# Optimization experiments

Hardware: AMD Instinct MI355X
Metric: run time of the kernel (lower is better)

The kernel has to match this reference:

```python
import jax, jax.numpy as jnp
import numpy as np

N = 50000
E = 800000


def gcn_conv(h_in, W, b, src, dst, n_nodes):
    # h_in: [N, Fin] -> linear transform first (PyG GCNConv default)
    h = h_in @ W  # [N, Fout]
    # add self loops
    loop = jnp.arange(n_nodes, dtype=src.dtype)
    s = jnp.concatenate([src, loop])
    d = jnp.concatenate([dst, loop])
    # symmetric normalization: deg computed on destination with unit edge weights
    deg = jax.ops.segment_sum(jnp.ones_like(s, dtype=h.dtype), d, num_segments=n_nodes)
    dinv = jnp.where(deg > 0, jax.lax.rsqrt(deg), 0.0)
    norm = dinv[s] * dinv[d]  # [E+N]
    # gather source features, scale, scatter-add to destinations
    msg = h[s] * norm[:, None]  # [E+N, Fout]
    out = jax.ops.segment_sum(msg, d, num_segments=n_nodes)
    return out + b


def setup_inputs() -> dict:
    key = jax.random.key(0)
    ks = jax.random.split(key, 6)
    x = jax.random.normal(ks[0], (N, 256), dtype=jnp.float32)
    edge_index = jax.random.randint(ks[1], (2, E), 0, N, dtype=jnp.int64)
    # Glorot-style scaling for weights
    W1 = jax.random.normal(ks[2], (256, 128), dtype=jnp.float32) * (1.0 / np.sqrt(256))
    b1 = jnp.zeros((128,), dtype=jnp.float32)
    W2 = jax.random.normal(ks[3], (128, 64), dtype=jnp.float32) * (1.0 / np.sqrt(128))
    b2 = jnp.zeros((64,), dtype=jnp.float32)
    return {"x": x, "edge_index": edge_index, "W1": W1, "b1": b1, "W2": W2, "b2": b2}


def reference(x, edge_index, W1, b1, W2, b2):
    src, dst = edge_index[0], edge_index[1]
    h = gcn_conv(x, W1, b1, src, dst, N)
    h = jax.nn.relu(h)
    out = gcn_conv(h, W2, b2, src, dst, N)
    return out
```

## Files before the change

kernel.cpp:

```cpp
#include <hip/hip_runtime.h>

#define FIN   256
#define F1    128
#define F2    64

typedef _Float16 f16x8 __attribute__((ext_vector_type(8)));
typedef _Float16 f16x4 __attribute__((ext_vector_type(4)));
typedef float    f32x4 __attribute__((ext_vector_type(4)));

#define BUCKET_SHIFT 7
#define BUCKET_W     128
#define MAXBUCK      512
#define CAP          2560
#define CHUNK        2048

__global__ __launch_bounds__(256) void prep(const float* __restrict__ W1,
                                            const float* __restrict__ W2,
                                            _Float16* __restrict__ WT1,
                                            _Float16* __restrict__ WT2,
                                            int* __restrict__ bcur_pad) {
    int b = blockIdx.x;
    if (b == 0) {
        for (int i = threadIdx.x; i < MAXBUCK; i += 256) bcur_pad[i * 16] = i * CAP;
        return;
    }
    int idx = (b - 1) * 256 + threadIdx.x;
    if (idx < FIN * F1) {
        int k = idx / F1, n = idx % F1;
        WT1[(size_t)n * FIN + k] = (_Float16)W1[idx];
    } else {
        int j = idx - FIN * F1;
        if (j < F1 * F2) {
            int k = j / F2, n = j % F2;
            WT2[(size_t)n * F1 + k] = (_Float16)W2[j];
        }
    }
}

__global__ __launch_bounds__(512) void bucket_fill(const int* __restrict__ src,
                                                   const int* __restrict__ dst,
                                                   int* __restrict__ bcur_pad,
                                                   unsigned* __restrict__ ebuf, int E) {
    __shared__ int h[MAXBUCK];
    __shared__ int base[MAXBUCK];
    for (int i = threadIdx.x; i < MAXBUCK; i += 512) h[i] = 0;
    __syncthreads();
    int cbase = blockIdx.x * CHUNK;
    int lim   = min(cbase + CHUNK, E);
    for (int e = cbase + threadIdx.x; e < lim; e += 512)
        atomicAdd(&h[dst[e] >> BUCKET_SHIFT], 1);
    __syncthreads();
    for (int i = threadIdx.x; i < MAXBUCK; i += 512) {
        int c = h[i];
        base[i] = c ? atomicAdd(&bcur_pad[i * 16], c) : 0;
        h[i] = 0;
    }
    __syncthreads();
    for (int e = cbase + threadIdx.x; e < lim; e += 512) {
        int d = dst[e], b = d >> BUCKET_SHIFT;
        int r = atomicAdd(&h[b], 1);
        int pos = base[b] + r;
        if (pos < (b + 1) * CAP)
            ebuf[pos] = ((unsigned)src[e] << BUCKET_SHIFT) | (unsigned)(d & (BUCKET_W - 1));
    }
}

__global__ __launch_bounds__(512) void csr_build(const unsigned* __restrict__ ebuf,
                                                 const int* __restrict__ bcur_pad,
                                                 unsigned* __restrict__ rowinfo,
                                                 float* __restrict__ dinv,
                                                 int* __restrict__ csr, int n) {
    __shared__ int cnt[BUCKET_W];
    __shared__ int sbuf[2][BUCKET_W];
    __shared__ int lcur[BUCKET_W];
    int k = blockIdx.x, t = threadIdx.x;
    int ebeg = k * CAP;
    int cntk = min(bcur_pad[k * 16] - ebeg, CAP);
    if (t < BUCKET_W) cnt[t] = 0;
    __syncthreads();
    for (int e = t; e < cntk; e += 512)
        atomicAdd(&cnt[ebuf[ebeg + e] & (BUCKET_W - 1)], 1);
    __syncthreads();
    int myc = (t < BUCKET_W) ? cnt[t] : 0;
    if (t < BUCKET_W) sbuf[0][t] = myc;
    __syncthreads();
    int cur = 0;
    for (int off = 1; off < BUCKET_W; off <<= 1) {
        if (t < BUCKET_W) {
            int v = sbuf[cur][t];
            if (t >= off) v += sbuf[cur][t - off];
            sbuf[cur ^ 1][t] = v;
        }
        cur ^= 1;
        __syncthreads();
    }
    if (t < BUCKET_W) {
        int excl = sbuf[cur][t] - myc;
        int beg  = ebeg + excl;
        lcur[t] = beg;
        int node = (k << BUCKET_SHIFT) + t;
        if (node < n) {
            rowinfo[node] = ((unsigned)beg << 8) | (unsigned)min(myc, 255);
            dinv[node]    = rsqrtf((float)(myc + 1));
        }
    }
    __syncthreads();
    for (int e = t; e < cntk; e += 512) {
        unsigned ed = ebuf[ebeg + e];
        int pos = atomicAdd(&lcur[ed & (BUCKET_W - 1)], 1);
        csr[pos] = (int)(ed >> BUCKET_SHIFT);
    }
}

template <int BN, int K, typename AT>
__global__ __launch_bounds__(256) void gemm_mfma(const AT* __restrict__ A,
                                                 const _Float16* __restrict__ WT,
                                                 const float* __restrict__ dinv,
                                                 _Float16* __restrict__ Ch, int M) {
    constexpr int NB = BN / 16;
    constexpr int CH = K / 32;
    constexpr int KP = K + 8;
    __shared__ _Float16 Bs[BN][KP];

    int tid  = threadIdx.x;
    int wave = tid >> 6, lane = tid & 63;
    int col  = lane & 15, kg = lane >> 4;
    int row0 = blockIdx.x * 64;
    int arow = row0 + wave * 16 + col;
    bool rowok = arow < M;

    float4 paf[sizeof(AT) == 4 ? 2 * CH : 1];
    f16x8  pah[sizeof(AT) == 2 ? CH : 1];
    const AT* Ab = A + (size_t)arow * K + kg * 8;
    if constexpr (sizeof(AT) == 4) {
#pragma unroll
        for (int c = 0; c < CH; ++c) {
            paf[2 * c]     = make_float4(0.f, 0.f, 0.f, 0.f);
            paf[2 * c + 1] = make_float4(0.f, 0.f, 0.f, 0.f);
            if (rowok) {
                paf[2 * c]     = *(const float4*)((const float*)Ab + c * 32);
                paf[2 * c + 1] = *(const float4*)((const float*)Ab + c * 32 + 4);
            }
        }
    } else {
#pragma unroll
        for (int c = 0; c < CH; ++c) {
            pah[c] = (f16x8){0, 0, 0, 0, 0, 0, 0, 0};
            if (rowok) pah[c] = *(const f16x8*)((const _Float16*)Ab + c * 32);
        }
    }

    constexpr int TOT = BN * K / 8;
#pragma unroll
    for (int l = 0; l < TOT / 256; ++l) {
        int u  = l * 256 + tid;
        int r  = u / (K / 8);
        int c8 = u % (K / 8);
        *(f16x8*)&Bs[r][c8 * 8] = *(const f16x8*)&WT[(size_t)r * K + c8 * 8];
    }
    __syncthreads();

    f32x4 acc[NB];
#pragma unroll
    for (int j = 0; j < NB; ++j) acc[j] = (f32x4){0.f, 0.f, 0.f, 0.f};

#pragma unroll
    for (int c = 0; c < CH; ++c) {
        f16x8 a;
        if constexpr (sizeof(AT) == 4) {
            float4 lo = paf[2 * c], hi = paf[2 * c + 1];
            a[0] = (_Float16)lo.x; a[1] = (_Float16)lo.y;
            a[2] = (_Float16)lo.z; a[3] = (_Float16)lo.w;
            a[4] = (_Float16)hi.x; a[5] = (_Float16)hi.y;
            a[6] = (_Float16)hi.z; a[7] = (_Float16)hi.w;
        } else {
            a = pah[c];
        }
#pragma unroll
        for (int j = 0; j < NB; ++j) {
            f16x8 b = *(const f16x8*)&Bs[j * 16 + col][c * 32 + kg * 8];
            acc[j] = __builtin_amdgcn_mfma_f32_16x16x32_f16(a, b, acc[j], 0, 0, 0);
        }
    }

    int rbase = row0 + wave * 16 + kg * 4;
#pragma unroll
    for (int r = 0; r < 4; ++r) {
        int m = rbase + r;
        if (m < M) {
            float dv = dinv[m];
#pragma unroll
            for (int j = 0; j < NB; ++j)
                Ch[(size_t)m * BN + j * 16 + col] = (_Float16)(dv * acc[j][r]);
        }
    }
}

template <int F, bool RELU, typename OutT>
__global__ __launch_bounds__(256) void aggregate(const _Float16* __restrict__ Hs,
                                                 const unsigned* __restrict__ rowinfo,
                                                 const int* __restrict__ csr,
                                                 const float* __restrict__ dinv,
                                                 const float* __restrict__ bias,
                                                 OutT* __restrict__ out, int n) {
    constexpr int LPG = F / 8;
    int gid = (blockIdx.x * blockDim.x + threadIdx.x) / LPG;
    int sub = threadIdx.x & (LPG - 1);
    if (gid >= n) return;
    const int col = sub * 8;

    float a[8];
    {
        f16x8 h = *(const f16x8*)&Hs[(size_t)gid * F + col];
#pragma unroll
        for (int i = 0; i < 8; ++i) a[i] = (float)h[i];
    }

    unsigned ri = rowinfo[gid];
    int e   = (int)(ri >> 8);
    int end = e + (int)(ri & 255u);

    for (; e + 8 <= end; e += 8) {
        int s0 = csr[e + 0], s1 = csr[e + 1], s2 = csr[e + 2], s3 = csr[e + 3];
        int s4 = csr[e + 4], s5 = csr[e + 5], s6 = csr[e + 6], s7 = csr[e + 7];
        f16x8 v0 = *(const f16x8*)&Hs[(size_t)s0 * F + col];
        f16x8 v1 = *(const f16x8*)&Hs[(size_t)s1 * F + col];
        f16x8 v2 = *(const f16x8*)&Hs[(size_t)s2 * F + col];
        f16x8 v3 = *(const f16x8*)&Hs[(size_t)s3 * F + col];
        f16x8 v4 = *(const f16x8*)&Hs[(size_t)s4 * F + col];
        f16x8 v5 = *(const f16x8*)&Hs[(size_t)s5 * F + col];
        f16x8 v6 = *(const f16x8*)&Hs[(size_t)s6 * F + col];
        f16x8 v7 = *(const f16x8*)&Hs[(size_t)s7 * F + col];
#pragma unroll
        for (int i = 0; i < 8; ++i) {
            a[i] += (((float)v0[i] + (float)v1[i]) + ((float)v2[i] + (float)v3[i]))
                  + (((float)v4[i] + (float)v5[i]) + ((float)v6[i] + (float)v7[i]));
        }
    }
    for (; e + 4 <= end; e += 4) {
        int s0 = csr[e + 0], s1 = csr[e + 1], s2 = csr[e + 2], s3 = csr[e + 3];
        f16x8 v0 = *(const f16x8*)&Hs[(size_t)s0 * F + col];
        f16x8 v1 = *(const f16x8*)&Hs[(size_t)s1 * F + col];
        f16x8 v2 = *(const f16x8*)&Hs[(size_t)s2 * F + col];
        f16x8 v3 = *(const f16x8*)&Hs[(size_t)s3 * F + col];
#pragma unroll
        for (int i = 0; i < 8; ++i)
            a[i] += ((float)v0[i] + (float)v1[i]) + ((float)v2[i] + (float)v3[i]);
    }
    for (; e < end; ++e) {
        int s = csr[e];
        f16x8 v = *(const f16x8*)&Hs[(size_t)s * F + col];
#pragma unroll
        for (int i = 0; i < 8; ++i) a[i] += (float)v[i];
    }

    float dv = dinv[gid];
    float4 bb0 = *(const float4*)&bias[col];
    float4 bb1 = *(const float4*)&bias[col + 4];
    float o[8];
    o[0] = dv * a[0] + bb0.x; o[1] = dv * a[1] + bb0.y;
    o[2] = dv * a[2] + bb0.z; o[3] = dv * a[3] + bb0.w;
    o[4] = dv * a[4] + bb1.x; o[5] = dv * a[5] + bb1.y;
    o[6] = dv * a[6] + bb1.z; o[7] = dv * a[7] + bb1.w;
    if (RELU) {
#pragma unroll
        for (int i = 0; i < 8; ++i) o[i] = fmaxf(o[i], 0.f);
    }
    if constexpr (sizeof(OutT) == 2) {
        f16x8 ov;
#pragma unroll
        for (int i = 0; i < 8; ++i) ov[i] = (_Float16)o[i];
        *(f16x8*)&out[(size_t)gid * F + col] = ov;
    } else {
        float4 ov0 = make_float4(o[0], o[1], o[2], o[3]);
        float4 ov1 = make_float4(o[4], o[5], o[6], o[7]);
        *(float4*)&out[(size_t)gid * F + col]     = ov0;
        *(float4*)&out[(size_t)gid * F + col + 4] = ov1;
    }
}

extern "C" void kernel_launch(void* const* d_in, const int* in_sizes, int n_in,
                              void* d_out, int out_size, void* d_ws, size_t ws_size,
                              hipStream_t stream) {
    const float* x  = (const float*)d_in[0];
    const int*   ei = (const int*)d_in[1];
    const float* W1 = (const float*)d_in[2];
    const float* b1 = (const float*)d_in[3];
    const float* W2 = (const float*)d_in[4];
    const float* b2 = (const float*)d_in[5];
    float* out = (float*)d_out;

    const int N = in_sizes[0] / FIN;
    const int E = in_sizes[1] / 2;
    const int* src = ei;
    const int* dst = ei + E;

    char* w = (char*)d_ws;
    auto alloc = [&](size_t bytes) {
        void* p = (void*)w;
        w += (bytes + 255) & ~(size_t)255;
        return p;
    };
    float*    dinv     = (float*)alloc((size_t)N * 4);
    unsigned* rowinfo  = (unsigned*)alloc((size_t)N * 4);
    int*      csr      = (int*)alloc((size_t)MAXBUCK * CAP * 4);
    int*      bcur_pad = (int*)alloc((size_t)MAXBUCK * 16 * 4);
    unsigned* ebuf     = (unsigned*)alloc((size_t)MAXBUCK * CAP * 4);
    _Float16* WT1      = (_Float16*)alloc((size_t)FIN * F1 * 2);
    _Float16* WT2      = (_Float16*)alloc((size_t)F1 * F2 * 2);
    _Float16* Hs1      = (_Float16*)alloc((size_t)N * F1 * 2);
    _Float16* X2h      = (_Float16*)alloc((size_t)N * F1 * 2);

    const int nbuck  = (N + BUCKET_W - 1) >> BUCKET_SHIFT;
    const int nchunk = (E + CHUNK - 1) / CHUNK;
    const int nprep  = 1 + (FIN * F1 + F1 * F2 + 255) / 256;

    prep<<<nprep, 256, 0, stream>>>(W1, W2, WT1, WT2, bcur_pad);
    bucket_fill<<<nchunk, 512, 0, stream>>>(src, dst, bcur_pad, ebuf, E);
    csr_build<<<nbuck, 512, 0, stream>>>(ebuf, bcur_pad, rowinfo, dinv, csr, N);

    gemm_mfma<F1, FIN, float><<<(N + 63) / 64, 256, 0, stream>>>(x, WT1, dinv, Hs1, N);
    {
        int blocks = (int)(((size_t)N * (F1 / 8) + 255) / 256);
        aggregate<F1, true, _Float16><<<blocks, 256, 0, stream>>>(Hs1, rowinfo, csr, dinv, b1, X2h, N);
    }

    gemm_mfma<F2, F1, _Float16><<<(N + 63) / 64, 256, 0, stream>>>(X2h, WT2, dinv, Hs1, N);
    {
        int blocks = (int)(((size_t)N * (F2 / 8) + 255) / 256);
        aggregate<F2, false, float><<<blocks, 256, 0, stream>>>(Hs1, rowinfo, csr, dinv, b2, out, N);
    }
}
```

Measured before the change: 109.8 us.

## Fuse layer-1 aggregation with layer-2 GEMM in one kernel

Replaces the separate layer-1 aggregate kernel and layer-2 MFMA GEMM with a single kernel. Each 64-node block aggregates neighbours into shared memory, applies bias and ReLU, then multiplies by W2 with MFMA and writes the dinv-scaled fp16 result. This avoids writing and re-reading the N x 128 fp16 intermediate and saves one kernel launch. In exchange, each block uses more shared memory and runs the gather and the GEMM back to back without overlap.

```diff
diff --git a/kernel.cpp b/kernel.cpp
--- a/kernel.cpp
+++ b/kernel.cpp
@@ -192,6 +192,125 @@
 #pragma unroll
             for (int j = 0; j < NB; ++j)
                 Ch[(size_t)m * BN + j * 16 + col] = (_Float16)(dv * acc[j][r]);
+        }
+    }
+}
+
+__global__ __launch_bounds__(256) void agg1_gemm2(const _Float16* __restrict__ Hs,
+                                                  const unsigned* __restrict__ rowinfo,
+                                                  const int* __restrict__ csr,
+                                                  const float* __restrict__ dinv,
+                                                  const float* __restrict__ bias,
+                                                  const _Float16* __restrict__ WT2,
+                                                  _Float16* __restrict__ Hs2, int n) {
+    constexpr int KP = F1 + 8;
+    __shared__ _Float16 Xs[64][KP];
+    __shared__ _Float16 Ws[F2][KP];
+
+    int tid = threadIdx.x;
+
+    f16x8 wreg[4];
+#pragma unroll
+    for (int l = 0; l < 4; ++l)
+        wreg[l] = *(const f16x8*)&WT2[(l * 256 + tid) * 8];
+
+    int node0 = blockIdx.x * 64;
+    int sub = tid & 15;
+    int grp = tid >> 4;
+    const int col = sub * 8;
+
+#pragma unroll
+    for (int r = 0; r < 4; ++r) {
+        int nloc = r * 16 + grp;
+        int gid  = node0 + nloc;
+        f16x8 t = (f16x8){0, 0, 0, 0, 0, 0, 0, 0};
+        if (gid < n) {
+            float a[8];
+            {
+                f16x8 h = *(const f16x8*)&Hs[(size_t)gid * F1 + col];
+#pragma unroll
+                for (int i = 0; i < 8; ++i) a[i] = (float)h[i];
+            }
+            unsigned ri = rowinfo[gid];
+            int e   = (int)(ri >> 8);
+            int end = e + (int)(ri & 255u);
+            for (; e + 8 <= end; e += 8) {
+                int s0 = csr[e + 0], s1 = csr[e + 1], s2 = csr[e + 2], s3 = csr[e + 3];
+                int s4 = csr[e + 4], s5 = csr[e + 5], s6 = csr[e + 6], s7 = csr[e + 7];
+                f16x8 v0 = *(const f16x8*)&Hs[(size_t)s0 * F1 + col];
+                f16x8 v1 = *(const f16x8*)&Hs[(size_t)s1 * F1 + col];
+                f16x8 v2 = *(const f16x8*)&Hs[(size_t)s2 * F1 + col];
+                f16x8 v3 = *(const f16x8*)&Hs[(size_t)s3 * F1 + col];
+                f16x8 v4 = *(const f16x8*)&Hs[(size_t)s4 * F1 + col];
+                f16x8 v5 = *(const f16x8*)&Hs[(size_t)s5 * F1 + col];
+                f16x8 v6 = *(const f16x8*)&Hs[(size_t)s6 * F1 + col];
+                f16x8 v7 = *(const f16x8*)&Hs[(size_t)s7 * F1 + col];
+#pragma unroll
+                for (int i = 0; i < 8; ++i)
+                    a[i] += (((float)v0[i] + (float)v1[i]) + ((float)v2[i] + (float)v3[i]))
+                          + (((float)v4[i] + (float)v5[i]) + ((float)v6[i] + (float)v7[i]));
+            }
+            for (; e + 4 <= end; e += 4) {
+                int s0 = csr[e + 0], s1 = csr[e + 1], s2 = csr[e + 2], s3 = csr[e + 3];
+                f16x8 v0 = *(const f16x8*)&Hs[(size_t)s0 * F1 + col];
+                f16x8 v1 = *(const f16x8*)&Hs[(size_t)s1 * F1 + col];
+                f16x8 v2 = *(const f16x8*)&Hs[(size_t)s2 * F1 + col];
+                f16x8 v3 = *(const f16x8*)&Hs[(size_t)s3 * F1 + col];
+#pragma unroll
+                for (int i = 0; i < 8; ++i)
+                    a[i] += ((float)v0[i] + (float)v1[i]) + ((float)v2[i] + (float)v3[i]);
+            }
+            for (; e < end; ++e) {
+                int s = csr[e];
+                f16x8 v = *(const f16x8*)&Hs[(size_t)s * F1 + col];
+#pragma unroll
+                for (int i = 0; i < 8; ++i) a[i] += (float)v[i];
+            }
+            float dv = dinv[gid];
+            float4 bb0 = *(const float4*)&bias[col];
+            float4 bb1 = *(const float4*)&bias[col + 4];
+            float o[8];
+            o[0] = dv * a[0] + bb0.x; o[1] = dv * a[1] + bb0.y;
+            o[2] = dv * a[2] + bb0.z; o[3] = dv * a[3] + bb0.w;
+            o[4] = dv * a[4] + bb1.x; o[5] = dv * a[5] + bb1.y;
+            o[6] = dv * a[6] + bb1.z; o[7] = dv * a[7] + bb1.w;
+#pragma unroll
+            for (int i = 0; i < 8; ++i) t[i] = (_Float16)fmaxf(o[i], 0.f);
+        }
+        *(f16x8*)&Xs[nloc][col] = t;
+    }
+
+#pragma unroll
+    for (int l = 0; l < 4; ++l) {
+        int u  = l * 256 + tid;
+        int rr = u >> 4, c8 = u & 15;
+        *(f16x8*)&Ws[rr][c8 * 8] = wreg[l];
+    }
+    __syncthreads();
+
+    int wave = tid >> 6, lane = tid & 63;
+    int mcol = lane & 15, kg = lane >> 4;
+    f32x4 acc[4];
+#pragma unroll
+    for (int j = 0; j < 4; ++j) acc[j] = (f32x4){0.f, 0.f, 0.f, 0.f};
+#pragma unroll
+    for (int c = 0; c < 4; ++c) {
+        f16x8 a = *(const f16x8*)&Xs[wave * 16 + mcol][c * 32 + kg * 8];
+#pragma unroll
+        for (int j = 0; j < 4; ++j) {
+            f16x8 b = *(const f16x8*)&Ws[j * 16 + mcol][c * 32 + kg * 8];
+            acc[j] = __builtin_amdgcn_mfma_f32_16x16x32_f16(a, b, acc[j], 0, 0, 0);
+        }
+    }
+    int rbase = node0 + wave * 16 + kg * 4;
+#pragma unroll
+    for (int r = 0; r < 4; ++r) {
+        int m = rbase + r;
+        if (m < n) {
+            float dv = dinv[m];
+#pragma unroll
+            for (int j = 0; j < 4; ++j)
+                Hs2[(size_t)m * F2 + j * 16 + mcol] = (_Float16)(dv * acc[j][r]);
         }
     }
 }
@@ -309,7 +428,7 @@
     _Float16* WT1      = (_Float16*)alloc((size_t)FIN * F1 * 2);
     _Float16* WT2      = (_Float16*)alloc((size_t)F1 * F2 * 2);
     _Float16* Hs1      = (_Float16*)alloc((size_t)N * F1 * 2);
-    _Float16* X2h      = (_Float16*)alloc((size_t)N * F1 * 2);
+    _Float16* Hs2      = (_Float16*)alloc((size_t)N * F2 * 2);
 
     const int nbuck  = (N + BUCKET_W - 1) >> BUCKET_SHIFT;
     const int nchunk = (E + CHUNK - 1) / CHUNK;
@@ -320,14 +439,11 @@
     csr_build<<<nbuck, 512, 0, stream>>>(ebuf, bcur_pad, rowinfo, dinv, csr, N);
 
     gemm_mfma<F1, FIN, float><<<(N + 63) / 64, 256, 0, stream>>>(x, WT1, dinv, Hs1, N);
-    {
-        int blocks = (int)(((size_t)N * (F1 / 8) + 255) / 256);
-        aggregate<F1, true, _Float16><<<blocks, 256, 0, stream>>>(Hs1, rowinfo, csr, dinv, b1, X2h, N);
-    }
-
-    gemm_mfma<F2, F1, _Float16><<<(N + 63) / 64, 256, 0, stream>>>(X2h, WT2, dinv, Hs1, N);
+
+    agg1_gemm2<<<(N + 63) / 64, 256, 0, stream>>>(Hs1, rowinfo, csr, dinv, b1, WT2, Hs2, N);
+
     {
         int blocks = (int)(((size_t)N * (F2 / 8) + 255) / 256);
-        aggregate<F2, false, float><<<blocks, 256, 0, stream>>>(Hs1, rowinfo, csr, dinv, b2, out, N);
-    }
-}
+        aggregate<F2, false, float><<<blocks, 256, 0, stream>>>(Hs2, rowinfo, csr, dinv, b2, out, N);
+    }
+}
```

Result: faster. 105.2 us (-4.2%).
